# Optimization experiments

Measured on AMD Instinct MI355X. Metric: run time of the kernel, lower is better.

The kernel has to match this reference:

```python
import jax, jax.numpy as jnp
import numpy as np

HIDDEN = 1024
HEADS = 16
HEAD_DIM = HIDDEN // HEADS


def setup_inputs() -> dict:
    key = jax.random.key(0)
    k_x, k_wqkv, k_bqkv, k_wo, k_bo = jax.random.split(key, 5)
    s = 1.0 / np.sqrt(HIDDEN)
    return {
        "x": jax.random.normal(k_x, (2, 2048, HIDDEN), dtype=jnp.float32),
        "w_qkv": jax.random.uniform(k_wqkv, (HIDDEN, 3 * HIDDEN), jnp.float32, -s, s),
        "b_qkv": jax.random.uniform(k_bqkv, (3 * HIDDEN,), jnp.float32, -s, s),
        "w_out": jax.random.uniform(k_wo, (HIDDEN, HIDDEN), jnp.float32, -s, s),
        "b_out": jax.random.uniform(k_bo, (HIDDEN,), jnp.float32, -s, s),
    }


def reference(x, w_qkv, b_qkv, w_out, b_out):
    b, s, h = x.shape
    scale = jnp.float32(HEAD_DIM) ** 0.5
    qkv = x @ w_qkv + b_qkv                      # [b, s, 3h]
    qkv = qkv.reshape(b, s, 3, HEADS, HEAD_DIM)
    q, k, v = jnp.moveaxis(qkv, 2, 0)            # each [b, s, heads, head_dim]
    # scores: [b, heads, s, s]
    attn = jnp.einsum("bqhd,bkhd->bhqk", q, k) / scale
    attn = jax.nn.softmax(attn, axis=-1)
    out = jnp.einsum("bhqk,bkhd->bqhd", attn, v).reshape(b, s, h)
    return out @ w_out + b_out
```

## Files before the change

### kernel.cpp

```cpp
#include <hip/hip_runtime.h>
#include <math.h>

#define SEQ 2048
#define NH 16
#define HD 64
#define NB 2
#define HID 1024

typedef unsigned short ushort_t;
using short8 = __attribute__((ext_vector_type(8))) short;
using f32x4  = __attribute__((ext_vector_type(4))) float;

__device__ __forceinline__ ushort_t f2bf(float f) {
  union { float f; unsigned u; } v; v.f = f;
  unsigned r = v.u + 0x7fffu + ((v.u >> 16) & 1u);
  return (ushort_t)(r >> 16);
}

__device__ __forceinline__ short8 ld8u(const ushort_t* p) {
  short8 r;
  const short4 a = *(const short4*)p;
  const short4 b = *(const short4*)(p + 4);
  r[0] = a.x; r[1] = a.y; r[2] = a.z; r[3] = a.w;
  r[4] = b.x; r[5] = b.y; r[6] = b.z; r[7] = b.w;
  return r;
}

__device__ __forceinline__ void glds16(const ushort_t* g, ushort_t* l) {
  __builtin_amdgcn_global_load_lds((const __attribute__((address_space(1))) void*)g,
                                   (__attribute__((address_space(3))) void*)l, 16, 0, 0);
}

__global__ __launch_bounds__(256)
void f2b_k(const float* __restrict__ in, ushort_t* __restrict__ out) {
  const int i = (blockIdx.x * 256 + threadIdx.x) * 8;
  float4 a = *(const float4*)(in + i);
  float4 b = *(const float4*)(in + i + 4);
  ushort_t o[8] = { f2bf(a.x), f2bf(a.y), f2bf(a.z), f2bf(a.w),
                    f2bf(b.x), f2bf(b.y), f2bf(b.z), f2bf(b.w) };
  *(uint4*)(out + i) = *(const uint4*)o;
}

__global__ __launch_bounds__(256)
void wtrans_k(const float* __restrict__ w, ushort_t* __restrict__ wt, int K, int N) {
  __shared__ ushort_t tile[32][33];
  const int t = threadIdx.x;
  const int k0 = blockIdx.y << 5, n0 = blockIdx.x << 5;
  const int kr = t >> 3, nc4 = (t & 7) << 2;
  float4 a = *(const float4*)&w[(size_t)(k0 + kr) * N + n0 + nc4];
  tile[nc4 + 0][kr] = f2bf(a.x);
  tile[nc4 + 1][kr] = f2bf(a.y);
  tile[nc4 + 2][kr] = f2bf(a.z);
  tile[nc4 + 3][kr] = f2bf(a.w);
  __syncthreads();
  const int nr = t >> 3, kc4 = (t & 7) << 2;
  ushort4 o;
  o.x = tile[nr][kc4 + 0]; o.y = tile[nr][kc4 + 1];
  o.z = tile[nr][kc4 + 2]; o.w = tile[nr][kc4 + 3];
  *(ushort4*)&wt[(size_t)(n0 + nr) * K + k0 + kc4] = o;
}

__global__ __launch_bounds__(256)
void vtrans_k(const ushort_t* __restrict__ in, ushort_t* __restrict__ out) {
  __shared__ ushort_t tile[32][34];
  const int t = threadIdx.x;
  const int s0 = blockIdx.x << 5, d0 = blockIdx.y << 5, bh = blockIdx.z;
  const size_t base = (size_t)bh * SEQ * HD;
  const int r = t >> 3, c4 = (t & 7) << 2;
  ushort4 v = *(const ushort4*)&in[base + (size_t)(s0 + r) * HD + d0 + c4];
  tile[c4 + 0][r] = v.x; tile[c4 + 1][r] = v.y;
  tile[c4 + 2][r] = v.z; tile[c4 + 3][r] = v.w;
  __syncthreads();
  ushort4 o;
  o.x = tile[r][c4 + 0]; o.y = tile[r][c4 + 1];
  o.z = tile[r][c4 + 2]; o.w = tile[r][c4 + 3];
  *(ushort4*)&out[base + (size_t)(d0 + r) * SEQ + s0 + c4] = o;
}

#define QSCL 0.18033688f

template<int EPI>
__global__ __launch_bounds__(256)
void gemm_bf16(const ushort_t* __restrict__ A, const ushort_t* __restrict__ BT,
               const float* __restrict__ bias, float* __restrict__ Cf,
               ushort_t* __restrict__ qb, ushort_t* __restrict__ kb,
               ushort_t* __restrict__ vb)
{
  __shared__ ushort_t As[128 * 32];
  __shared__ ushort_t Bs[128 * 32];
  const int t = threadIdx.x;
  const int w = t >> 6, lane = t & 63;
  const int m0 = blockIdx.y << 7, n0 = blockIdx.x << 7;
  const int wm = (w >> 1) << 6, wn = (w & 1) << 6;

  f32x4 acc[4][4];
#pragma unroll
  for (int i = 0; i < 4; ++i)
#pragma unroll
    for (int j = 0; j < 4; ++j) acc[i][j] = (f32x4){0.f, 0.f, 0.f, 0.f};

  const ushort_t* gA = A + (size_t)(m0 + (w << 5) + (lane >> 2)) * HID + ((lane & 3) << 3);
  const ushort_t* gB = BT + (size_t)(n0 + (w << 5) + (lane >> 2)) * HID + ((lane & 3) << 3);
  ushort_t* lA = As + (w << 5) * 32;
  ushort_t* lB = Bs + (w << 5) * 32;
  const int ra = (lane & 15) * 32 + ((lane >> 4) << 3);

  for (int k0 = 0; k0 < HID; k0 += 32) {
    __syncthreads();
    glds16(gA + k0, lA);
    glds16(gA + k0 + 16 * HID, lA + 16 * 32);
    glds16(gB + k0, lB);
    glds16(gB + k0 + 16 * HID, lB + 16 * 32);
    __syncthreads();
    short8 af[4], bf[4];
#pragma unroll
    for (int mt = 0; mt < 4; ++mt) af[mt] = *(const short8*)&As[(wm + mt * 16) * 32 + ra];
#pragma unroll
    for (int nt = 0; nt < 4; ++nt) bf[nt] = *(const short8*)&Bs[(wn + nt * 16) * 32 + ra];
#pragma unroll
    for (int mt = 0; mt < 4; ++mt)
#pragma unroll
      for (int nt = 0; nt < 4; ++nt)
        acc[mt][nt] = __builtin_amdgcn_mfma_f32_16x16x32_bf16(af[mt], bf[nt], acc[mt][nt], 0, 0, 0);
  }

  if (EPI == 0) {
#pragma unroll
    for (int nt = 0; nt < 4; ++nt) {
      const int n = n0 + wn + nt * 16 + (lane & 15);
      const float bv = bias[n];
#pragma unroll
      for (int mt = 0; mt < 4; ++mt) {
        const int m = m0 + wm + mt * 16 + ((lane >> 4) << 2);
#pragma unroll
        for (int r = 0; r < 4; ++r)
          Cf[(size_t)(m + r) * HID + n] = acc[mt][nt][r] + bv;
      }
    }
  } else {
    const int which = n0 >> 10;
    const float scl = (which == 0) ? QSCL : 1.0f;
    ushort_t* outb = (which == 0) ? qb : (which == 1) ? kb : vb;
#pragma unroll
    for (int nt = 0; nt < 4; ++nt) {
      const int ng = n0 + wn + nt * 16 + (lane & 15);
      const int nloc = ng & 1023;
      const int h = nloc >> 6, d = nloc & 63;
      const float bv = bias[ng];
#pragma unroll
      for (int mt = 0; mt < 4; ++mt) {
        const int m = m0 + wm + mt * 16 + ((lane >> 4) << 2);
        const int b = m >> 11, s0 = m & 2047;
        ushort_t* dst = outb + ((size_t)(b * NH + h) * SEQ + s0) * HD + d;
#pragma unroll
        for (int r = 0; r < 4; ++r)
          dst[(size_t)r * HD] = f2bf((acc[mt][nt][r] + bv) * scl);
      }
    }
  }
}

__global__ __launch_bounds__(256)
void attn_mfma(const ushort_t* __restrict__ qb, const ushort_t* __restrict__ kb,
               const ushort_t* __restrict__ vtb, ushort_t* __restrict__ awb)
{
  __shared__ ushort_t Ks[2][64 * 64];
  __shared__ ushort_t Vs[2][64 * 64];
  __shared__ ushort_t Ps[4][16 * 68];

  const int t = threadIdx.x, w = t >> 6, lane = t & 63;
  const int q0 = blockIdx.x << 6, bh = blockIdx.y;
  const size_t base = (size_t)bh * SEQ * HD;

  const ushort_t* qp = qb + base + (size_t)(q0 + (w << 4) + (lane & 15)) * HD + ((lane >> 4) << 3);
  const short8 qf0 = *(const short8*)qp;
  const short8 qf1 = *(const short8*)(qp + 32);

  const int sr  = t >> 3;
  const int sc8 = (t & 7) << 3;
  const int swz = (sr & 7) << 3;
  const int sw0 = sr * 64 + (sc8 ^ swz);
  const int sw1 = (sr + 32) * 64 + (sc8 ^ swz);
  const ushort_t* kg  = kb  + base + (size_t)sr * HD + sc8;
  const ushort_t* kg2 = kg  + (size_t)32 * HD;
  const ushort_t* vg  = vtb + base + (size_t)sr * SEQ + sc8;
  const ushort_t* vg2 = vg  + (size_t)32 * SEQ;

  uint4 kr0 = *(const uint4*)kg,  kr1 = *(const uint4*)kg2;
  uint4 vr0 = *(const uint4*)vg,  vr1 = *(const uint4*)vg2;
  *(uint4*)&Ks[0][sw0] = kr0;  *(uint4*)&Ks[0][sw1] = kr1;
  *(uint4*)&Vs[0][sw0] = vr0;  *(uint4*)&Vs[0][sw1] = vr1;
  kr0 = *(const uint4*)(kg  + 64 * HD);  kr1 = *(const uint4*)(kg2 + 64 * HD);
  vr0 = *(const uint4*)(vg  + 64);       vr1 = *(const uint4*)(vg2 + 64);
  asm volatile("s_waitcnt lgkmcnt(0)" ::: "memory");
  __builtin_amdgcn_sched_barrier(0);
  __builtin_amdgcn_s_barrier();
  __builtin_amdgcn_sched_barrier(0);

  f32x4 O[4];
  float mrow[4], lrow[4];
#pragma unroll
  for (int i = 0; i < 4; ++i) { O[i] = (f32x4){0.f, 0.f, 0.f, 0.f}; mrow[i] = -3.0e38f; lrow[i] = 0.f; }

  const int rb  = (lane & 15) * 64;
  const int sl0 = (((lane >> 4)    ) << 3) ^ ((lane & 7) << 3);
  const int sl1 = (((lane >> 4) + 4) << 3) ^ ((lane & 7) << 3);
  ushort_t* ps = &Ps[w][0];
  const int q68 = (lane & 15) * 68 + ((lane >> 4) << 3);

  for (int kt = 0; kt < SEQ / 64; ++kt) {
    const int p = kt & 1;

    f32x4 S[4];
#pragma unroll
    for (int nt = 0; nt < 4; ++nt) {
      const ushort_t* kp = &Ks[p][nt * 1024 + rb];
      short8 k0v = *(const short8*)(kp + sl0);
      short8 k1v = *(const short8*)(kp + sl1);
      S[nt] = (f32x4){0.f, 0.f, 0.f, 0.f};
      S[nt] = __builtin_amdgcn_mfma_f32_16x16x32_bf16(qf0, k0v, S[nt], 0, 0, 0);
      S[nt] = __builtin_amdgcn_mfma_f32_16x16x32_bf16(qf1, k1v, S[nt], 0, 0, 0);
    }

    float tmv[4];
    bool need = false;
#pragma unroll
    for (int r = 0; r < 4; ++r) {
      float tm = fmaxf(fmaxf(S[0][r], S[1][r]), fmaxf(S[2][r], S[3][r]));
      tm = fmaxf(tm, __shfl_xor(tm, 1));
      tm = fmaxf(tm, __shfl_xor(tm, 2));
      tm = fmaxf(tm, __shfl_xor(tm, 4));
      tm = fmaxf(tm, __shfl_xor(tm, 8));
      tmv[r] = tm;
      need = need || (tm > mrow[r] + 11.5f);
    }
    if (__any(need ? 1 : 0)) {
#pragma unroll
      for (int r = 0; r < 4; ++r) {
        const float mnew = fmaxf(mrow[r], tmv[r]);
        const float al = exp2f(mrow[r] - mnew);
        mrow[r] = mnew;
        float ts = 0.f;
#pragma unroll
        for (int nt = 0; nt < 4; ++nt) { float pv = exp2f(S[nt][r] - mnew); S[nt][r] = pv; ts += pv; }
        lrow[r] = lrow[r] * al + ts;
#pragma unroll
        for (int nt = 0; nt < 4; ++nt) O[nt][r] *= al;
      }
    } else {
#pragma unroll
      for (int r = 0; r < 4; ++r) {
        float ts = 0.f;
#pragma unroll
        for (int nt = 0; nt < 4; ++nt) { float pv = exp2f(S[nt][r] - mrow[r]); S[nt][r] = pv; ts += pv; }
        lrow[r] += ts;
      }
    }

#pragma unroll
    for (int nt = 0; nt < 4; ++nt)
#pragma unroll
      for (int r = 0; r < 4; ++r)
        ps[(((lane >> 4) << 2) + r) * 68 + nt * 16 + (lane & 15)] = f2bf(S[nt][r]);
    asm volatile("s_waitcnt lgkmcnt(0)" ::: "memory");
    __builtin_amdgcn_sched_barrier(0);

    short8 pa0 = ld8u(ps + q68);
    short8 pa1 = ld8u(ps + q68 + 32);

#pragma unroll
    for (int nt = 0; nt < 4; ++nt) {
      const ushort_t* vp = &Vs[p][nt * 1024 + rb];
      short8 v0 = *(const short8*)(vp + sl0);
      short8 v1 = *(const short8*)(vp + sl1);
      O[nt] = __builtin_amdgcn_mfma_f32_16x16x32_bf16(pa0, v0, O[nt], 0, 0, 0);
      O[nt] = __builtin_amdgcn_mfma_f32_16x16x32_bf16(pa1, v1, O[nt], 0, 0, 0);
    }

    *(uint4*)&Ks[p ^ 1][sw0] = kr0;  *(uint4*)&Ks[p ^ 1][sw1] = kr1;
    *(uint4*)&Vs[p ^ 1][sw0] = vr0;  *(uint4*)&Vs[p ^ 1][sw1] = vr1;
    const int ktn = (kt + 2 <= 31) ? (kt + 2) : 31;
    kr0 = *(const uint4*)(kg  + ktn * 64 * HD);
    kr1 = *(const uint4*)(kg2 + ktn * 64 * HD);
    vr0 = *(const uint4*)(vg  + ktn * 64);
    vr1 = *(const uint4*)(vg2 + ktn * 64);
    asm volatile("s_waitcnt lgkmcnt(0)" ::: "memory");
    __builtin_amdgcn_sched_barrier(0);
    __builtin_amdgcn_s_barrier();
    __builtin_amdgcn_sched_barrier(0);
  }

  const int b = bh >> 4, h = bh & 15;
#pragma unroll
  for (int r = 0; r < 4; ++r) {
    float ls = lrow[r];
    ls += __shfl_xor(ls, 1);
    ls += __shfl_xor(ls, 2);
    ls += __shfl_xor(ls, 4);
    ls += __shfl_xor(ls, 8);
    const float inv = 1.0f / ls;
    const int q = q0 + (w << 4) + ((lane >> 4) << 2) + r;
    ushort_t* dst = awb + (size_t)(b * SEQ + q) * HID + h * HD + (lane & 15);
#pragma unroll
    for (int nt = 0; nt < 4; ++nt)
      dst[nt * 16] = f2bf(O[nt][r] * inv);
  }
}

extern "C" void kernel_launch(void* const* d_in, const int* in_sizes, int n_in,
                              void* d_out, int out_size, void* d_ws, size_t ws_size,
                              hipStream_t stream)
{
  const float* x     = (const float*)d_in[0];
  const float* w_qkv = (const float*)d_in[1];
  const float* b_qkv = (const float*)d_in[2];
  const float* w_out = (const float*)d_in[3];
  const float* b_out = (const float*)d_in[4];

  ushort_t* ws    = (ushort_t*)d_ws;
  ushort_t* xb    = ws;
  ushort_t* wqkvT = xb + (size_t)4096 * 1024;
  ushort_t* woutT = wqkvT + (size_t)3072 * 1024;
  ushort_t* qbuf  = woutT + (size_t)1024 * 1024;
  ushort_t* kbuf  = qbuf + (size_t)32 * 2048 * 64;
  ushort_t* vbuf  = kbuf + (size_t)32 * 2048 * 64;
  ushort_t* vtbuf = vbuf + (size_t)32 * 2048 * 64;
  ushort_t* awb   = vtbuf + (size_t)32 * 2048 * 64;

  f2b_k<<<2048, 256, 0, stream>>>(x, xb);
  wtrans_k<<<dim3(96, 32), 256, 0, stream>>>(w_qkv, wqkvT, HID, 3 * HID);
  wtrans_k<<<dim3(32, 32), 256, 0, stream>>>(w_out, woutT, HID, HID);

  gemm_bf16<1><<<dim3(24, 32), 256, 0, stream>>>(xb, wqkvT, b_qkv, nullptr,
                                                 qbuf, kbuf, vbuf);

  vtrans_k<<<dim3(64, 2, 32), 256, 0, stream>>>(vbuf, vtbuf);

  attn_mfma<<<dim3(32, 32), 256, 0, stream>>>(qbuf, kbuf, vtbuf, awb);

  gemm_bf16<0><<<dim3(8, 32), 256, 0, stream>>>(awb, woutT, b_out, (float*)d_out,
                                                nullptr, nullptr, nullptr);
}
```

Measured before the change: 256.1 us.

## Transpose QK^T MFMA so each lane owns one query row in softmax

```diff
diff --git a/kernel.cpp b/kernel.cpp
--- a/kernel.cpp
+++ b/kernel.cpp
@@ -1,4 +1,5 @@
 #include <hip/hip_runtime.h>
+#include <hip/hip_bf16.h>
 #include <math.h>
 
 #define SEQ 2048
@@ -11,19 +12,22 @@
 using short8 = __attribute__((ext_vector_type(8))) short;
 using f32x4  = __attribute__((ext_vector_type(4))) float;
 
+#if __has_builtin(__builtin_amdgcn_exp2f)
+#define EXP2 __builtin_amdgcn_exp2f
+#else
+#define EXP2 exp2f
+#endif
+
 __device__ __forceinline__ ushort_t f2bf(float f) {
   union { float f; unsigned u; } v; v.f = f;
   unsigned r = v.u + 0x7fffu + ((v.u >> 16) & 1u);
   return (ushort_t)(r >> 16);
 }
 
-__device__ __forceinline__ short8 ld8u(const ushort_t* p) {
-  short8 r;
-  const short4 a = *(const short4*)p;
-  const short4 b = *(const short4*)(p + 4);
-  r[0] = a.x; r[1] = a.y; r[2] = a.z; r[3] = a.w;
-  r[4] = b.x; r[5] = b.y; r[6] = b.z; r[7] = b.w;
-  return r;
+__device__ __forceinline__ unsigned pk2(float a, float b) {
+  union { __hip_bfloat162 h; unsigned u; } v;
+  v.h = __float22bfloat162_rn(make_float2(a, b));
+  return v.u;
 }
 
 __device__ __forceinline__ void glds16(const ushort_t* g, ushort_t* l) {
@@ -166,13 +170,14 @@
 {
   __shared__ ushort_t Ks[2][64 * 64];
   __shared__ ushort_t Vs[2][64 * 64];
-  __shared__ ushort_t Ps[4][16 * 68];
+  __shared__ ushort_t Ps[4][16 * 72];
 
   const int t = threadIdx.x, w = t >> 6, lane = t & 63;
+  const int g = lane >> 4, qi = lane & 15;
   const int q0 = blockIdx.x << 6, bh = blockIdx.y;
   const size_t base = (size_t)bh * SEQ * HD;
 
-  const ushort_t* qp = qb + base + (size_t)(q0 + (w << 4) + (lane & 15)) * HD + ((lane >> 4) << 3);
+  const ushort_t* qp = qb + base + (size_t)(q0 + (w << 4) + qi) * HD + (g << 3);
   const short8 qf0 = *(const short8*)qp;
   const short8 qf1 = *(const short8*)(qp + 32);
 
@@ -198,15 +203,18 @@
   __builtin_amdgcn_sched_barrier(0);
 
   f32x4 O[4];
-  float mrow[4], lrow[4];
-#pragma unroll
-  for (int i = 0; i < 4; ++i) { O[i] = (f32x4){0.f, 0.f, 0.f, 0.f}; mrow[i] = -3.0e38f; lrow[i] = 0.f; }
-
-  const int rb  = (lane & 15) * 64;
-  const int sl0 = (((lane >> 4)    ) << 3) ^ ((lane & 7) << 3);
-  const int sl1 = (((lane >> 4) + 4) << 3) ^ ((lane & 7) << 3);
+#pragma unroll
+  for (int i = 0; i < 4; ++i) O[i] = (f32x4){0.f, 0.f, 0.f, 0.f};
+  float mq = 0.f;
+  float lrow = 0.f;
+
+  const int rb  = qi * 64;
+  const int sl0 = ((g    ) << 3) ^ ((qi & 7) << 3);
+  const int sl1 = ((g + 4) << 3) ^ ((qi & 7) << 3);
   ushort_t* ps = &Ps[w][0];
-  const int q68 = (lane & 15) * 68 + ((lane >> 4) << 3);
+  const int pw  = qi * 72 + (g << 2);
+  const int pr0 = qi * 72 + (g << 3);
+  const int pr1 = pr0 + 32;
 
   for (int kt = 0; kt < SEQ / 64; ++kt) {
     const int p = kt & 1;
@@ -218,55 +226,47 @@
       short8 k0v = *(const short8*)(kp + sl0);
       short8 k1v = *(const short8*)(kp + sl1);
       S[nt] = (f32x4){0.f, 0.f, 0.f, 0.f};
-      S[nt] = __builtin_amdgcn_mfma_f32_16x16x32_bf16(qf0, k0v, S[nt], 0, 0, 0);
-      S[nt] = __builtin_amdgcn_mfma_f32_16x16x32_bf16(qf1, k1v, S[nt], 0, 0, 0);
-    }
-
-    float tmv[4];
-    bool need = false;
-#pragma unroll
-    for (int r = 0; r < 4; ++r) {
-      float tm = fmaxf(fmaxf(S[0][r], S[1][r]), fmaxf(S[2][r], S[3][r]));
-      tm = fmaxf(tm, __shfl_xor(tm, 1));
-      tm = fmaxf(tm, __shfl_xor(tm, 2));
-      tm = fmaxf(tm, __shfl_xor(tm, 4));
-      tm = fmaxf(tm, __shfl_xor(tm, 8));
-      tmv[r] = tm;
-      need = need || (tm > mrow[r] + 11.5f);
-    }
-    if (__any(need ? 1 : 0)) {
+      S[nt] = __builtin_amdgcn_mfma_f32_16x16x32_bf16(k0v, qf0, S[nt], 0, 0, 0);
+      S[nt] = __builtin_amdgcn_mfma_f32_16x16x32_bf16(k1v, qf1, S[nt], 0, 0, 0);
+    }
+
+    float pm = fmaxf(fmaxf(fmaxf(S[0][0], S[0][1]), fmaxf(S[0][2], S[0][3])),
+                     fmaxf(fmaxf(S[1][0], S[1][1]), fmaxf(S[1][2], S[1][3])));
+    pm = fmaxf(pm, fmaxf(fmaxf(fmaxf(S[2][0], S[2][1]), fmaxf(S[2][2], S[2][3])),
+                         fmaxf(fmaxf(S[3][0], S[3][1]), fmaxf(S[3][2], S[3][3]))));
+    if (__any((pm > mq + 11.5f) ? 1 : 0)) {
+      float rm = pm;
+      rm = fmaxf(rm, __shfl_xor(rm, 16));
+      rm = fmaxf(rm, __shfl_xor(rm, 32));
+      const float mnew = fmaxf(mq, rm);
+      const float al = EXP2(mq - mnew);
+      mq = mnew;
+      lrow *= al;
 #pragma unroll
       for (int r = 0; r < 4; ++r) {
-        const float mnew = fmaxf(mrow[r], tmv[r]);
-        const float al = exp2f(mrow[r] - mnew);
-        mrow[r] = mnew;
-        float ts = 0.f;
-#pragma unroll
-        for (int nt = 0; nt < 4; ++nt) { float pv = exp2f(S[nt][r] - mnew); S[nt][r] = pv; ts += pv; }
-        lrow[r] = lrow[r] * al + ts;
-#pragma unroll
-        for (int nt = 0; nt < 4; ++nt) O[nt][r] *= al;
+        const float alr = __shfl(al, (g << 2) + r);
+#pragma unroll
+        for (int nt = 0; nt < 4; ++nt) O[nt][r] *= alr;
       }
-    } else {
-#pragma unroll
-      for (int r = 0; r < 4; ++r) {
-        float ts = 0.f;
-#pragma unroll
-        for (int nt = 0; nt < 4; ++nt) { float pv = exp2f(S[nt][r] - mrow[r]); S[nt][r] = pv; ts += pv; }
-        lrow[r] += ts;
-      }
-    }
-
-#pragma unroll
-    for (int nt = 0; nt < 4; ++nt)
-#pragma unroll
-      for (int r = 0; r < 4; ++r)
-        ps[(((lane >> 4) << 2) + r) * 68 + nt * 16 + (lane & 15)] = f2bf(S[nt][r]);
+    }
+
+    float ts = 0.f;
+#pragma unroll
+    for (int nt = 0; nt < 4; ++nt) {
+      const float p0 = EXP2(S[nt][0] - mq);
+      const float p1 = EXP2(S[nt][1] - mq);
+      const float p2 = EXP2(S[nt][2] - mq);
+      const float p3 = EXP2(S[nt][3] - mq);
+      ts += (p0 + p1) + (p2 + p3);
+      uint2 u; u.x = pk2(p0, p1); u.y = pk2(p2, p3);
+      *(uint2*)&ps[pw + (nt << 4)] = u;
+    }
+    lrow += ts;
     asm volatile("s_waitcnt lgkmcnt(0)" ::: "memory");
     __builtin_amdgcn_sched_barrier(0);
 
-    short8 pa0 = ld8u(ps + q68);
-    short8 pa1 = ld8u(ps + q68 + 32);
+    const short8 pa0 = *(const short8*)&ps[pr0];
+    const short8 pa1 = *(const short8*)&ps[pr1];
 
 #pragma unroll
     for (int nt = 0; nt < 4; ++nt) {
@@ -290,20 +290,19 @@
     __builtin_amdgcn_sched_barrier(0);
   }
 
+  float ls = lrow;
+  ls += __shfl_xor(ls, 16);
+  ls += __shfl_xor(ls, 32);
+  const float inv = 1.0f / ls;
   const int b = bh >> 4, h = bh & 15;
 #pragma unroll
   for (int r = 0; r < 4; ++r) {
-    float ls = lrow[r];
-    ls += __shfl_xor(ls, 1);
-    ls += __shfl_xor(ls, 2);
-    ls += __shfl_xor(ls, 4);
-    ls += __shfl_xor(ls, 8);
-    const float inv = 1.0f / ls;
-    const int q = q0 + (w << 4) + ((lane >> 4) << 2) + r;
-    ushort_t* dst = awb + (size_t)(b * SEQ + q) * HID + h * HD + (lane & 15);
+    const float invr = __shfl(inv, (g << 2) + r);
+    const int q = q0 + (w << 4) + (g << 2) + r;
+    ushort_t* dst = awb + (size_t)(b * SEQ + q) * HID + h * HD + qi;
 #pragma unroll
     for (int nt = 0; nt < 4; ++nt)
-      dst[nt * 16] = f2bf(O[nt][r] * inv);
+      dst[nt * 16] = f2bf(O[nt][r] * invr);
   }
 }
 
```

New measurement: 217.9 us. 1.18x faster.
